# Optimization experiments

Measured on AMD Instinct MI355X. Metric: run time of the kernel, lower is better.

Reference implementation:

```python
import jax, jax.numpy as jnp
import numpy as np

B, N, D, P = 8, 256, 1024, 512  # batch, n_words, input_dim, proj_dim


def setup_inputs() -> dict:
    key = jax.random.key(0)
    ks = jax.random.split(key, 8)
    w = lambda k, shape: (jax.random.normal(k, shape, dtype=jnp.float32) * 0.02)
    return {
        "x": jax.random.normal(ks[0], (B, N, D), dtype=jnp.float32),
        # bigram path
        "Wl": w(ks[1], (P, D)), "bl": jnp.zeros((P,), jnp.float32),
        "Wr": w(ks[2], (P, D)),  # right proj has no bias
        "Wo": w(ks[3], (1, P)), "bo": jnp.zeros((1,), jnp.float32),
        # start builder: Linear -> ReLU -> Linear
        "Ws1": w(ks[4], (P, D)), "bs1": jnp.zeros((P,), jnp.float32),
        "Ws2": w(ks[5], (1, P)), "bs2": jnp.zeros((1,), jnp.float32),
        # end builder
        "We1": w(ks[6], (P, D)), "be1": jnp.zeros((P,), jnp.float32),
        "We2": w(ks[7], (1, P)), "be2": jnp.zeros((1,), jnp.float32),
    }


def reference(x, Wl, bl, Wr, Wo, bo, Ws1, bs1, Ws2, bs2, We1, be1, We2, be2):
    # start / end scorers: [B,N,1]
    start = jax.nn.relu(jnp.einsum('bnd,pd->bnp', x, Ws1) + bs1) @ Ws2.T + bs2
    end = jax.nn.relu(jnp.einsum('bnd,pd->bnp', x, We1) + be1) @ We2.T + be2
    # bigram projections: [B,N,P]
    left = jnp.einsum('bnd,pd->bnp', x, Wl) + bl
    right = jnp.einsum('bnd,pd->bnp', x, Wr)
    # outer-sum: proj[b,i,j,:] = left[b,j,:] + right[b,i,:]  -> [B,N,N,P]
    proj = jax.nn.relu(left[:, None, :, :] + right[:, :, None, :])
    bigram = jnp.einsum('bijp,qp->bijq', proj, Wo) + bo  # [B,N,N,1]
    return (bigram, start, end)
```

## Files before the change

kernel.cpp:

```cpp
#include <hip/hip_runtime.h>
#include <hip/hip_fp16.h>

typedef __attribute__((ext_vector_type(8))) short short8;
typedef __attribute__((ext_vector_type(4))) float f32x4;

constexpr int kB = 8;
constexpr int kN = 256;
constexpr int kD = 1024;
constexpr int kP = 512;
constexpr int kM = kB * kN;

__device__ __forceinline__ __half2 pk_max2(__half2 a, __half2 b) {
    unsigned ua = *reinterpret_cast<unsigned*>(&a);
    unsigned ub = *reinterpret_cast<unsigned*>(&b);
    unsigned ur;
    asm("v_pk_max_f16 %0, %1, %2" : "=v"(ur) : "v"(ua), "v"(ub));
    return *reinterpret_cast<__half2*>(&ur);
}

__global__ __launch_bounds__(256) void cvt_kernel(
    const float* __restrict__ x,
    const float* __restrict__ Wl, const float* __restrict__ Wr,
    const float* __restrict__ Ws1, const float* __restrict__ We1,
    const float* __restrict__ bs2, const float* __restrict__ be2,
    unsigned short* __restrict__ xb, unsigned short* __restrict__ wb,
    float* __restrict__ out_start, float* __restrict__ out_end)
{
    const int bid = blockIdx.x;
    if (bid >= 2048) {
        const int idx = (bid - 2048) * 256 + threadIdx.x;
        if (idx < 2048) out_start[idx] = bs2[0];
        else            out_end[idx - 2048] = be2[0];
        return;
    }
    const int g = bid * 256 + threadIdx.x;
    const float* src;
    unsigned short* dst;
    if (g < 262144) {
        src = x + (size_t)g * 8;
        dst = xb + (size_t)g * 8;
    } else {
        const int gg = g - 262144;
        const int w = gg >> 16;
        const int r = gg & 65535;
        const float* s = (w == 0) ? Wl : (w == 1) ? Wr : (w == 2) ? Ws1 : We1;
        src = s + (size_t)r * 8;
        dst = wb + ((size_t)w << 19) + (size_t)r * 8;
    }
    const float4 a = *reinterpret_cast<const float4*>(src);
    const float4 b = *reinterpret_cast<const float4*>(src + 4);
    const float v[8] = {a.x, a.y, a.z, a.w, b.x, b.y, b.z, b.w};
    short8 o;
#pragma unroll
    for (int i = 0; i < 8; ++i) {
        unsigned u = __float_as_uint(v[i]);
        u = u + 0x7FFF + ((u >> 16) & 1);
        o[i] = (short)(u >> 16);
    }
    *reinterpret_cast<short8*>(dst) = o;
}

__global__ __launch_bounds__(256) void proj_mfma(
    const unsigned short* __restrict__ xb, const unsigned short* __restrict__ wb,
    const float* __restrict__ bl, const float* __restrict__ bs1,
    const float* __restrict__ be1,
    const float* __restrict__ Ws2, const float* __restrict__ We2,
    __half* __restrict__ left_h, __half* __restrict__ right_h,
    float* __restrict__ out_start, float* __restrict__ out_end)
{
    __shared__ unsigned short As[2][64 * 64];
    __shared__ unsigned short Bs[2][64 * 64];

    const int r0 = blockIdx.x * 64;
    const int q0 = blockIdx.y * 64;
    const int z  = q0 >> 9;
    const int t = threadIdx.x, wid = t >> 6, lane = t & 63;
    const int wr = wid >> 1, wc = wid & 1;

    f32x4 acc[2][2] = {};

    const int srow0 = wid * 16 + (lane >> 3);
    const int scolh = ((lane & 7) ^ (lane >> 3)) << 3;
    const unsigned short* gA0 = xb + (size_t)(r0 + srow0) * kD + scolh;
    const unsigned short* gA1 = gA0 + (size_t)8 * kD;
    const unsigned short* gB0 = wb + (size_t)(q0 + srow0) * kD + scolh;
    const unsigned short* gB1 = gB0 + (size_t)8 * kD;

#define STAGE(buf, k0) do { \
    __builtin_amdgcn_global_load_lds( \
        (const __attribute__((address_space(1))) void*)(gA0 + (k0)), \
        (__attribute__((address_space(3))) void*)((char*)&As[buf][0] + wid * 2048), 16, 0, 0); \
    __builtin_amdgcn_global_load_lds( \
        (const __attribute__((address_space(1))) void*)(gA1 + (k0)), \
        (__attribute__((address_space(3))) void*)((char*)&As[buf][0] + wid * 2048 + 1024), 16, 0, 0); \
    __builtin_amdgcn_global_load_lds( \
        (const __attribute__((address_space(1))) void*)(gB0 + (k0)), \
        (__attribute__((address_space(3))) void*)((char*)&Bs[buf][0] + wid * 2048), 16, 0, 0); \
    __builtin_amdgcn_global_load_lds( \
        (const __attribute__((address_space(1))) void*)(gB1 + (k0)), \
        (__attribute__((address_space(3))) void*)((char*)&Bs[buf][0] + wid * 2048 + 1024), 16, 0, 0); \
} while (0)

    const int sw = (lane & 7) << 4;
    const int cb0 = (lane >> 4) * 16;
    const int rA = wr * 32 + (lane & 15);
    const int rB = wc * 32 + (lane & 15);

    STAGE(0, 0);
    __syncthreads();
    int cur = 0;
    for (int k0 = 0; k0 < kD; k0 += 64) {
        if (k0 + 64 < kD) STAGE(cur ^ 1, k0 + 64);
        short8 a[2][2], b[2][2];
#pragma unroll
        for (int m = 0; m < 2; ++m)
#pragma unroll
            for (int ks = 0; ks < 2; ++ks) {
                a[m][ks] = *reinterpret_cast<const short8*>(
                    (const char*)&As[cur][0] +
                    (rA + m * 16) * 128 + ((ks * 64 + cb0) ^ sw));
                b[m][ks] = *reinterpret_cast<const short8*>(
                    (const char*)&Bs[cur][0] +
                    (rB + m * 16) * 128 + ((ks * 64 + cb0) ^ sw));
            }
#pragma unroll
        for (int m = 0; m < 2; ++m)
#pragma unroll
            for (int n = 0; n < 2; ++n)
#pragma unroll
                for (int ks = 0; ks < 2; ++ks)
                    acc[m][n] = __builtin_amdgcn_mfma_f32_16x16x32_bf16(
                        a[m][ks], b[n][ks], acc[m][n], 0, 0, 0);
        __syncthreads();
        cur ^= 1;
    }
#undef STAGE

    int pcol[2]; float bq[2];
#pragma unroll
    for (int n = 0; n < 2; ++n) {
        pcol[n] = (q0 & 511) + wc * 32 + n * 16 + (lane & 15);
        bq[n] = (z == 0) ? bl[pcol[n]] : (z == 2) ? bs1[pcol[n]]
              : (z == 3) ? be1[pcol[n]] : 0.f;
    }
    if (z < 2) {
        __half* dst = (z == 0) ? left_h : right_h;
        const int bb = r0 >> 8;
        const int jbase = (r0 & 255) + wr * 32 + (lane >> 4) * 4;
#pragma unroll
        for (int n = 0; n < 2; ++n) {
            __half* drow = dst + (size_t)(bb * kP + pcol[n]) * kN;
#pragma unroll
            for (int m = 0; m < 2; ++m) {
                const f32x4 c = acc[m][n];
                __half2 h01 = __floats2half2_rn(c[0] + bq[n], c[1] + bq[n]);
                __half2 h23 = __floats2half2_rn(c[2] + bq[n], c[3] + bq[n]);
                uint2 u;
                u.x = *reinterpret_cast<unsigned*>(&h01);
                u.y = *reinterpret_cast<unsigned*>(&h23);
                *reinterpret_cast<uint2*>(&drow[jbase + m * 16]) = u;
            }
        }
    } else {
        const float* Wv = (z == 2) ? Ws2 : We2;
        float* outh = (z == 2) ? out_start : out_end;
        const float w0 = Wv[pcol[0]], w1 = Wv[pcol[1]];
        const int rbase = r0 + wr * 32 + (lane >> 4) * 4;
#pragma unroll
        for (int m = 0; m < 2; ++m) {
#pragma unroll
            for (int q = 0; q < 4; ++q) {
                float s = fmaxf(acc[m][0][q] + bq[0], 0.f) * w0 +
                          fmaxf(acc[m][1][q] + bq[1], 0.f) * w1;
                s += __shfl_xor(s, 1); s += __shfl_xor(s, 2);
                s += __shfl_xor(s, 4); s += __shfl_xor(s, 8);
                if ((lane & 15) == 0)
                    atomicAdd(&outh[rbase + m * 16 + q], s);
            }
        }
    }
}

__global__ __launch_bounds__(256) void bigram_kernel(
    const __half* __restrict__ left_h, const __half* __restrict__ right_h,
    const float* __restrict__ Wo, float* __restrict__ part)
{
    __shared__ __half ls[32][64];
    __shared__ __half2 rs2[32][64];
    __shared__ __half2 wos[32];

    const int bz = blockIdx.z, b = bz >> 4, pc = bz & 15;
    const int i0 = blockIdx.y * 64, j0 = blockIdx.x * 64;
    const int t = threadIdx.x, wid = t >> 6, lane = t & 63;
    const int tj = t & 15, ti = t >> 4;

    const __half* lbase = left_h  + (size_t)(b * kP + pc * 32) * kN;
    const __half* rbase = right_h + (size_t)(b * kP + pc * 32) * kN;

    {
        const int row = wid * 8 + (lane >> 3);
        __builtin_amdgcn_global_load_lds(
            (const __attribute__((address_space(1))) void*)
                (lbase + (size_t)row * kN + j0 + (lane & 7) * 8),
            (__attribute__((address_space(3))) void*)
                ((char*)&ls[0][0] + wid * 1024),
            16, 0, 0);
    }
    uint2 rload[2];
#pragma unroll
    for (int h = 0; h < 2; ++h) {
        const int idx = h * 256 + t, pp = idx >> 4, iq = idx & 15;
        rload[h] = *reinterpret_cast<const uint2*>(&rbase[(size_t)pp * kN + i0 + iq * 4]);
    }
    if (t < 32) wos[t] = __float2half2_rn(Wo[pc * 32 + t]);
#pragma unroll
    for (int h = 0; h < 2; ++h) {
        const int idx = h * 256 + t, pp = idx >> 4, iq = idx & 15;
        const unsigned lo = rload[h].x, hi = rload[h].y;
        uint4 d;
        d.x = (lo & 0xFFFFu) | (lo << 16);
        d.y = (lo >> 16)     | (lo & 0xFFFF0000u);
        d.z = (hi & 0xFFFFu) | (hi << 16);
        d.w = (hi >> 16)     | (hi & 0xFFFF0000u);
        *reinterpret_cast<uint4*>(&rs2[pp][iq * 4]) = d;
    }
    __syncthreads();

    const __half2 zero2 = __float2half2_rn(0.f);
    __half2 acc2[4][2];
#pragma unroll
    for (int ii = 0; ii < 4; ++ii)
#pragma unroll
        for (int jp = 0; jp < 2; ++jp) acc2[ii][jp] = zero2;

#pragma unroll 8
    for (int kk = 0; kk < 32; ++kk) {
        const __half2 wo2 = wos[kk];
        union { uint2 u; __half2 h[2]; } L;
        L.u = *reinterpret_cast<const uint2*>(&ls[kk][tj * 4]);
        union { uint4 u; __half2 h[4]; } R;
        R.u = *reinterpret_cast<const uint4*>(&rs2[kk][ti * 4]);
#pragma unroll
        for (int ii = 0; ii < 4; ++ii)
#pragma unroll
            for (int jp = 0; jp < 2; ++jp) {
                __half2 s = __hadd2(R.h[ii], L.h[jp]);
                s = pk_max2(s, zero2);
                acc2[ii][jp] = __hfma2(s, wo2, acc2[ii][jp]);
            }
    }

    float* po = part + (size_t)bz * 65536;
#pragma unroll
    for (int ii = 0; ii < 4; ++ii) {
        const float2 a = __half22float2(acc2[ii][0]);
        const float2 c = __half22float2(acc2[ii][1]);
        float4 o = {a.x, a.y, c.x, c.y};
        *reinterpret_cast<float4*>(&po[(i0 + ti * 4 + ii) * kN + j0 + tj * 4]) = o;
    }
}

__global__ __launch_bounds__(256) void reduce_kernel(
    const float* __restrict__ part, const float* __restrict__ bo,
    float* __restrict__ out)
{
    const int e4 = blockIdx.x * 256 + threadIdx.x;
    const int e = e4 * 4, b = e >> 16, r = e & 65535;
    const float bias = bo[0];
    float4 acc = {bias, bias, bias, bias};
#pragma unroll
    for (int k = 0; k < 16; ++k) {
        const float4 v = *reinterpret_cast<const float4*>(
            &part[(size_t)(b * 16 + k) * 65536 + r]);
        acc.x += v.x; acc.y += v.y; acc.z += v.z; acc.w += v.w;
    }
    *reinterpret_cast<float4*>(&out[e]) = acc;
}

extern "C" void kernel_launch(void* const* d_in, const int* in_sizes, int n_in,
                              void* d_out, int out_size, void* d_ws, size_t ws_size,
                              hipStream_t stream) {
    const float* x   = (const float*)d_in[0];
    const float* Wl  = (const float*)d_in[1];
    const float* bl  = (const float*)d_in[2];
    const float* Wr  = (const float*)d_in[3];
    const float* Wo  = (const float*)d_in[4];
    const float* bo  = (const float*)d_in[5];
    const float* Ws1 = (const float*)d_in[6];
    const float* bs1 = (const float*)d_in[7];
    const float* Ws2 = (const float*)d_in[8];
    const float* bs2 = (const float*)d_in[9];
    const float* We1 = (const float*)d_in[10];
    const float* be1 = (const float*)d_in[11];
    const float* We2 = (const float*)d_in[12];
    const float* be2 = (const float*)d_in[13];

    float* out        = (float*)d_out;
    float* out_bigram = out;
    float* out_start  = out + (size_t)kB * kN * kN;
    float* out_end    = out_start + (size_t)kB * kN;

    __half* left_h  = (__half*)d_ws;
    __half* right_h = left_h + (size_t)1048576;
    unsigned short* xb = (unsigned short*)((char*)d_ws + (size_t)4 * 1024 * 1024);
    unsigned short* wb = xb + (size_t)2097152;
    float* part = (float*)((char*)d_ws + (size_t)4 * 1024 * 1024);

    cvt_kernel<<<2064, 256, 0, stream>>>(
        x, Wl, Wr, Ws1, We1, bs2, be2, xb, wb, out_start, out_end);

    proj_mfma<<<dim3(32, 32), 256, 0, stream>>>(
        xb, wb, bl, bs1, be1, Ws2, We2, left_h, right_h, out_start, out_end);

    bigram_kernel<<<dim3(4, 4, 128), 256, 0, stream>>>(
        left_h, right_h, Wo, part);

    reduce_kernel<<<512, 256, 0, stream>>>(part, bo, out_bigram);
}
```

Before: 128.3 us.

## Replace bigram partial buffer and reduce kernel with atomic accumulation

The bigram kernel now splits the projection dimension into 8 chunks of 64 instead of 16 chunks of 32, and it atomically adds its fp32 results straight into the output. This removes the partial-sum buffer and the separate reduce kernel. The conversion kernel now pre-fills the whole output with the bias values so the atomics accumulate on top of them. In exchange, each output element takes 8 scalar float atomics, the per-block LDS footprint doubles, and the summation order is no longer deterministic.

Result: slower. 167.0 us (+30.2%).

```diff
diff --git a/kernel.cpp b/kernel.cpp
--- a/kernel.cpp
+++ b/kernel.cpp
@@ -22,15 +22,21 @@
     const float* __restrict__ x,
     const float* __restrict__ Wl, const float* __restrict__ Wr,
     const float* __restrict__ Ws1, const float* __restrict__ We1,
-    const float* __restrict__ bs2, const float* __restrict__ be2,
+    const float* __restrict__ bo, const float* __restrict__ bs2,
+    const float* __restrict__ be2,
     unsigned short* __restrict__ xb, unsigned short* __restrict__ wb,
-    float* __restrict__ out_start, float* __restrict__ out_end)
+    float* __restrict__ outall)
 {
     const int bid = blockIdx.x;
     if (bid >= 2048) {
         const int idx = (bid - 2048) * 256 + threadIdx.x;
-        if (idx < 2048) out_start[idx] = bs2[0];
-        else            out_end[idx - 2048] = be2[0];
+        const int e = idx * 4;
+        float bval;
+        if (e < 524288)      bval = bo[0];
+        else if (e < 526336) bval = bs2[0];
+        else                 bval = be2[0];
+        float4 v = {bval, bval, bval, bval};
+        *reinterpret_cast<float4*>(&outall[e]) = v;
         return;
     }
     const int g = bid * 256 + threadIdx.x;
@@ -183,38 +189,39 @@
 
 __global__ __launch_bounds__(256) void bigram_kernel(
     const __half* __restrict__ left_h, const __half* __restrict__ right_h,
-    const float* __restrict__ Wo, float* __restrict__ part)
+    const float* __restrict__ Wo, float* __restrict__ out)
 {
-    __shared__ __half ls[32][64];
-    __shared__ __half2 rs2[32][64];
-    __shared__ __half2 wos[32];
-
-    const int bz = blockIdx.z, b = bz >> 4, pc = bz & 15;
+    __shared__ __half ls[64][64];
+    __shared__ __half2 rs2[64][64];
+    __shared__ __half2 wos[64];
+
+    const int bz = blockIdx.z, b = bz >> 3, pc = bz & 7;
     const int i0 = blockIdx.y * 64, j0 = blockIdx.x * 64;
     const int t = threadIdx.x, wid = t >> 6, lane = t & 63;
     const int tj = t & 15, ti = t >> 4;
 
-    const __half* lbase = left_h  + (size_t)(b * kP + pc * 32) * kN;
-    const __half* rbase = right_h + (size_t)(b * kP + pc * 32) * kN;
-
-    {
-        const int row = wid * 8 + (lane >> 3);
+    const __half* lbase = left_h  + (size_t)(b * kP + pc * 64) * kN;
+    const __half* rbase = right_h + (size_t)(b * kP + pc * 64) * kN;
+
+#pragma unroll
+    for (int h = 0; h < 2; ++h) {
+        const int row = wid * 16 + h * 8 + (lane >> 3);
         __builtin_amdgcn_global_load_lds(
             (const __attribute__((address_space(1))) void*)
                 (lbase + (size_t)row * kN + j0 + (lane & 7) * 8),
             (__attribute__((address_space(3))) void*)
-                ((char*)&ls[0][0] + wid * 1024),
+                ((char*)&ls[0][0] + wid * 2048 + h * 1024),
             16, 0, 0);
     }
-    uint2 rload[2];
-#pragma unroll
-    for (int h = 0; h < 2; ++h) {
+    uint2 rload[4];
+#pragma unroll
+    for (int h = 0; h < 4; ++h) {
         const int idx = h * 256 + t, pp = idx >> 4, iq = idx & 15;
         rload[h] = *reinterpret_cast<const uint2*>(&rbase[(size_t)pp * kN + i0 + iq * 4]);
     }
-    if (t < 32) wos[t] = __float2half2_rn(Wo[pc * 32 + t]);
-#pragma unroll
-    for (int h = 0; h < 2; ++h) {
+    if (t < 64) wos[t] = __float2half2_rn(Wo[pc * 64 + t]);
+#pragma unroll
+    for (int h = 0; h < 4; ++h) {
         const int idx = h * 256 + t, pp = idx >> 4, iq = idx & 15;
         const unsigned lo = rload[h].x, hi = rload[h].y;
         uint4 d;
@@ -234,7 +241,7 @@
         for (int jp = 0; jp < 2; ++jp) acc2[ii][jp] = zero2;
 
 #pragma unroll 8
-    for (int kk = 0; kk < 32; ++kk) {
+    for (int kk = 0; kk < 64; ++kk) {
         const __half2 wo2 = wos[kk];
         union { uint2 u; __half2 h[2]; } L;
         L.u = *reinterpret_cast<const uint2*>(&ls[kk][tj * 4]);
@@ -250,31 +257,16 @@
             }
     }
 
-    float* po = part + (size_t)bz * 65536;
 #pragma unroll
     for (int ii = 0; ii < 4; ++ii) {
         const float2 a = __half22float2(acc2[ii][0]);
         const float2 c = __half22float2(acc2[ii][1]);
-        float4 o = {a.x, a.y, c.x, c.y};
-        *reinterpret_cast<float4*>(&po[(i0 + ti * 4 + ii) * kN + j0 + tj * 4]) = o;
-    }
-}
-
-__global__ __launch_bounds__(256) void reduce_kernel(
-    const float* __restrict__ part, const float* __restrict__ bo,
-    float* __restrict__ out)
-{
-    const int e4 = blockIdx.x * 256 + threadIdx.x;
-    const int e = e4 * 4, b = e >> 16, r = e & 65535;
-    const float bias = bo[0];
-    float4 acc = {bias, bias, bias, bias};
-#pragma unroll
-    for (int k = 0; k < 16; ++k) {
-        const float4 v = *reinterpret_cast<const float4*>(
-            &part[(size_t)(b * 16 + k) * 65536 + r]);
-        acc.x += v.x; acc.y += v.y; acc.z += v.z; acc.w += v.w;
-    }
-    *reinterpret_cast<float4*>(&out[e]) = acc;
+        float* row = out + ((size_t)b * kN + (i0 + ti * 4 + ii)) * kN + j0 + tj * 4;
+        atomicAdd(row + 0, a.x);
+        atomicAdd(row + 1, a.y);
+        atomicAdd(row + 2, c.x);
+        atomicAdd(row + 3, c.y);
+    }
 }
 
 extern "C" void kernel_launch(void* const* d_in, const int* in_sizes, int n_in,
@@ -304,16 +296,13 @@
     __half* right_h = left_h + (size_t)1048576;
     unsigned short* xb = (unsigned short*)((char*)d_ws + (size_t)4 * 1024 * 1024);
     unsigned short* wb = xb + (size_t)2097152;
-    float* part = (float*)((char*)d_ws + (size_t)4 * 1024 * 1024);
-
-    cvt_kernel<<<2064, 256, 0, stream>>>(
-        x, Wl, Wr, Ws1, We1, bs2, be2, xb, wb, out_start, out_end);
+
+    cvt_kernel<<<2564, 256, 0, stream>>>(
+        x, Wl, Wr, Ws1, We1, bo, bs2, be2, xb, wb, out);
 
     proj_mfma<<<dim3(32, 32), 256, 0, stream>>>(
         xb, wb, bl, bs1, be1, Ws2, We2, left_h, right_h, out_start, out_end);
 
-    bigram_kernel<<<dim3(4, 4, 128), 256, 0, stream>>>(
-        left_h, right_h, Wo, part);
-
-    reduce_kernel<<<512, 256, 0, stream>>>(part, bo, out_bigram);
-}
+    bigram_kernel<<<dim3(4, 4, 64), 256, 0, stream>>>(
+        left_h, right_h, Wo, out_bigram);
+}
```

## Fuse P-split reduction into bigram kernel, dropping partial buffer and reduce pass

Applied to the files above, without the earlier changes.

The bigram kernel now processes all 512 projection channels per block over a 32x32 output tile and writes the final biased result directly, eliminating the fp32 partial buffer and the separate reduce kernel. Right values are expanded with byte perms in registers instead of being pre-duplicated in shared memory. This removes a large round-trip of partial sums through global memory and one launch, at the cost of fewer blocks, a lower compute-to-LDS-load ratio, and fp16 accumulation over many more terms, which risks accuracy.

New measurement: 128.5 us. No clear change (+0.1%).

```diff
diff --git a/kernel.cpp b/kernel.cpp
--- a/kernel.cpp
+++ b/kernel.cpp
@@ -183,98 +183,81 @@
 
 __global__ __launch_bounds__(256) void bigram_kernel(
     const __half* __restrict__ left_h, const __half* __restrict__ right_h,
-    const float* __restrict__ Wo, float* __restrict__ part)
+    const float* __restrict__ Wo, const float* __restrict__ bo,
+    float* __restrict__ out)
 {
-    __shared__ __half ls[32][64];
-    __shared__ __half2 rs2[32][64];
-    __shared__ __half2 wos[32];
-
-    const int bz = blockIdx.z, b = bz >> 4, pc = bz & 15;
-    const int i0 = blockIdx.y * 64, j0 = blockIdx.x * 64;
+    __shared__ __half ls[512][32];
+    __shared__ __half rs[512][32];
+    __shared__ __half2 wos2[512];
+
+    const int j0 = blockIdx.x * 32, i0 = blockIdx.y * 32, b = blockIdx.z;
     const int t = threadIdx.x, wid = t >> 6, lane = t & 63;
     const int tj = t & 15, ti = t >> 4;
 
-    const __half* lbase = left_h  + (size_t)(b * kP + pc * 32) * kN;
-    const __half* rbase = right_h + (size_t)(b * kP + pc * 32) * kN;
-
-    {
-        const int row = wid * 8 + (lane >> 3);
+    const __half* lbase = left_h  + (size_t)b * kP * kN + j0;
+    const __half* rbase = right_h + (size_t)b * kP * kN + i0;
+
+#pragma unroll
+    for (int c = 0; c < 8; ++c) {
+        const int seg = c * 4 + wid;
+        const int row = seg * 16 + (lane >> 2);
+        const int jo  = (lane & 3) * 8;
         __builtin_amdgcn_global_load_lds(
             (const __attribute__((address_space(1))) void*)
-                (lbase + (size_t)row * kN + j0 + (lane & 7) * 8),
+                (lbase + (size_t)row * kN + jo),
             (__attribute__((address_space(3))) void*)
-                ((char*)&ls[0][0] + wid * 1024),
+                ((char*)&ls[0][0] + seg * 1024),
             16, 0, 0);
-    }
-    uint2 rload[2];
-#pragma unroll
-    for (int h = 0; h < 2; ++h) {
-        const int idx = h * 256 + t, pp = idx >> 4, iq = idx & 15;
-        rload[h] = *reinterpret_cast<const uint2*>(&rbase[(size_t)pp * kN + i0 + iq * 4]);
-    }
-    if (t < 32) wos[t] = __float2half2_rn(Wo[pc * 32 + t]);
-#pragma unroll
-    for (int h = 0; h < 2; ++h) {
-        const int idx = h * 256 + t, pp = idx >> 4, iq = idx & 15;
-        const unsigned lo = rload[h].x, hi = rload[h].y;
-        uint4 d;
-        d.x = (lo & 0xFFFFu) | (lo << 16);
-        d.y = (lo >> 16)     | (lo & 0xFFFF0000u);
-        d.z = (hi & 0xFFFFu) | (hi << 16);
-        d.w = (hi >> 16)     | (hi & 0xFFFF0000u);
-        *reinterpret_cast<uint4*>(&rs2[pp][iq * 4]) = d;
-    }
+        __builtin_amdgcn_global_load_lds(
+            (const __attribute__((address_space(1))) void*)
+                (rbase + (size_t)row * kN + jo),
+            (__attribute__((address_space(3))) void*)
+                ((char*)&rs[0][0] + seg * 1024),
+            16, 0, 0);
+    }
+    wos2[t]       = __float2half2_rn(Wo[t]);
+    wos2[t + 256] = __float2half2_rn(Wo[t + 256]);
     __syncthreads();
 
-    const __half2 zero2 = __float2half2_rn(0.f);
-    __half2 acc2[4][2];
-#pragma unroll
-    for (int ii = 0; ii < 4; ++ii)
-#pragma unroll
-        for (int jp = 0; jp < 2; ++jp) acc2[ii][jp] = zero2;
+    const unsigned* lsu = (const unsigned*)&ls[0][0];
+    const unsigned* rsu = (const unsigned*)&rs[0][0];
+
+    __half2 accA[2] = {__half2{0,0}, __half2{0,0}};
+    __half2 accB[2] = {__half2{0,0}, __half2{0,0}};
 
 #pragma unroll 8
-    for (int kk = 0; kk < 32; ++kk) {
-        const __half2 wo2 = wos[kk];
-        union { uint2 u; __half2 h[2]; } L;
-        L.u = *reinterpret_cast<const uint2*>(&ls[kk][tj * 4]);
-        union { uint4 u; __half2 h[4]; } R;
-        R.u = *reinterpret_cast<const uint4*>(&rs2[kk][ti * 4]);
-#pragma unroll
-        for (int ii = 0; ii < 4; ++ii)
-#pragma unroll
-            for (int jp = 0; jp < 2; ++jp) {
-                __half2 s = __hadd2(R.h[ii], L.h[jp]);
-                s = pk_max2(s, zero2);
-                acc2[ii][jp] = __hfma2(s, wo2, acc2[ii][jp]);
-            }
-    }
-
-    float* po = part + (size_t)bz * 65536;
-#pragma unroll
-    for (int ii = 0; ii < 4; ++ii) {
-        const float2 a = __half22float2(acc2[ii][0]);
-        const float2 c = __half22float2(acc2[ii][1]);
-        float4 o = {a.x, a.y, c.x, c.y};
-        *reinterpret_cast<float4*>(&po[(i0 + ti * 4 + ii) * kN + j0 + tj * 4]) = o;
-    }
-}
-
-__global__ __launch_bounds__(256) void reduce_kernel(
-    const float* __restrict__ part, const float* __restrict__ bo,
-    float* __restrict__ out)
-{
-    const int e4 = blockIdx.x * 256 + threadIdx.x;
-    const int e = e4 * 4, b = e >> 16, r = e & 65535;
+    for (int kk = 0; kk < 512; kk += 2) {
+        const unsigned L0 = lsu[kk * 16 + tj];
+        const unsigned L1 = lsu[(kk + 1) * 16 + tj];
+        const unsigned R0 = rsu[kk * 16 + ti];
+        const unsigned R1 = rsu[(kk + 1) * 16 + ti];
+        const __half2 w0 = wos2[kk], w1 = wos2[kk + 1];
+
+        const unsigned r00 = __builtin_amdgcn_perm(R0, R0, 0x01000100);
+        const unsigned r01 = __builtin_amdgcn_perm(R0, R0, 0x03020302);
+        const unsigned r10 = __builtin_amdgcn_perm(R1, R1, 0x01000100);
+        const unsigned r11 = __builtin_amdgcn_perm(R1, R1, 0x03020302);
+
+        const __half2 l0 = *reinterpret_cast<const __half2*>(&L0);
+        const __half2 l1 = *reinterpret_cast<const __half2*>(&L1);
+        const __half2 zero2 = __half2{0, 0};
+
+        accA[0] = __hfma2(pk_max2(__hadd2(*reinterpret_cast<const __half2*>(&r00), l0), zero2), w0, accA[0]);
+        accA[1] = __hfma2(pk_max2(__hadd2(*reinterpret_cast<const __half2*>(&r01), l0), zero2), w0, accA[1]);
+        accB[0] = __hfma2(pk_max2(__hadd2(*reinterpret_cast<const __half2*>(&r10), l1), zero2), w1, accB[0]);
+        accB[1] = __hfma2(pk_max2(__hadd2(*reinterpret_cast<const __half2*>(&r11), l1), zero2), w1, accB[1]);
+    }
+
     const float bias = bo[0];
-    float4 acc = {bias, bias, bias, bias};
-#pragma unroll
-    for (int k = 0; k < 16; ++k) {
-        const float4 v = *reinterpret_cast<const float4*>(
-            &part[(size_t)(b * 16 + k) * 65536 + r]);
-        acc.x += v.x; acc.y += v.y; acc.z += v.z; acc.w += v.w;
-    }
-    *reinterpret_cast<float4*>(&out[e]) = acc;
+#pragma unroll
+    for (int ii = 0; ii < 2; ++ii) {
+        const float2 fa = __half22float2(accA[ii]);
+        const float2 fb = __half22float2(accB[ii]);
+        float2 o = {fa.x + fb.x + bias, fa.y + fb.y + bias};
+        const int i = i0 + ti * 2 + ii;
+        *reinterpret_cast<float2*>(
+            &out[((size_t)b * kN + i) * kN + j0 + tj * 2]) = o;
+    }
 }
 
 extern "C" void kernel_launch(void* const* d_in, const int* in_sizes, int n_in,
@@ -304,7 +287,6 @@
     __half* right_h = left_h + (size_t)1048576;
     unsigned short* xb = (unsigned short*)((char*)d_ws + (size_t)4 * 1024 * 1024);
     unsigned short* wb = xb + (size_t)2097152;
-    float* part = (float*)((char*)d_ws + (size_t)4 * 1024 * 1024);
 
     cvt_kernel<<<2064, 256, 0, stream>>>(
         x, Wl, Wr, Ws1, We1, bs2, be2, xb, wb, out_start, out_end);
@@ -312,8 +294,6 @@
     proj_mfma<<<dim3(32, 32), 256, 0, stream>>>(
         xb, wb, bl, bs1, be1, Ws2, We2, left_h, right_h, out_start, out_end);
 
-    bigram_kernel<<<dim3(4, 4, 128), 256, 0, stream>>>(
-        left_h, right_h, Wo, part);
-
-    reduce_kernel<<<512, 256, 0, stream>>>(part, bo, out_bigram);
-}
+    bigram_kernel<<<dim3(8, 8, 8), 256, 0, stream>>>(
+        left_h, right_h, Wo, bo, out_bigram);
+}
```
